# Optimization experiments

Hardware: AMD Instinct MI355X
Metric: run time of the kernel (lower is better)

The kernel has to match this reference:

```python
import jax, jax.numpy as jnp
import numpy as np

BSZ, T, ENC, HID = 128, 512, 128, 128


def setup_inputs() -> dict:
    key = jax.random.key(0)
    ks = jax.random.split(key, 8)
    encoder_output = jax.random.normal(ks[0], (BSZ, T, ENC), dtype=jnp.float32)
    lengths = jax.random.randint(ks[1], (BSZ,), 4, T + 1)
    mask = (jnp.arange(T)[None, :] < lengths[:, None]).astype(jnp.int32)
    s = 1.0 / np.sqrt(HID)  # torch LSTM init range
    W_ih = jax.random.uniform(ks[2], (4 * HID, ENC), jnp.float32, -s, s)
    W_hh = jax.random.uniform(ks[3], (4 * HID, HID), jnp.float32, -s, s)
    b_ih = jax.random.uniform(ks[4], (4 * HID,), jnp.float32, -s, s)
    b_hh = jax.random.uniform(ks[5], (4 * HID,), jnp.float32, -s, s)
    s2 = 1.0 / np.sqrt(HID + ENC)  # torch Linear init range
    fc_w = jax.random.uniform(ks[6], (1, HID + ENC), jnp.float32, -s2, s2)
    fc_b = jax.random.uniform(ks[7], (1,), jnp.float32, -s2, s2)
    return {"encoder_output": encoder_output, "mask": mask, "W_ih": W_ih,
            "W_hh": W_hh, "b_ih": b_ih, "b_hh": b_hh, "fc_w": fc_w, "fc_b": fc_b}


def _lstm_last(src, W_ih, W_hh, b_ih, b_hh):
    # src: [N, 3, E] -> last hidden state [N, H]; torch gate order i,f,g,o
    N = src.shape[0]
    H = W_hh.shape[1]
    h0 = jnp.zeros((N, H), src.dtype)
    c0 = jnp.zeros((N, H), src.dtype)

    def step(carry, x):
        h, c = carry
        gates = x @ W_ih.T + h @ W_hh.T + b_ih + b_hh
        i, f, g, o = jnp.split(gates, 4, axis=-1)
        c = jax.nn.sigmoid(f) * c + jax.nn.sigmoid(i) * jnp.tanh(g)
        h = jax.nn.sigmoid(o) * jnp.tanh(c)
        return (h, c), None

    (h, _), _ = jax.lax.scan(step, (h0, c0), jnp.swapaxes(src, 0, 1))
    return h


def reference(encoder_output, mask, W_ih, W_hh, b_ih, b_hh, fc_w, fc_b):
    B, Tn, E = encoder_output.shape
    H = W_hh.shape[1]
    lengths = jnp.sum(mask, axis=1)                       # [B]
    J = Tn - 3                                            # number of window starts
    # his_turn_states: encoder_output zeroed beyond each length
    states = encoder_output * mask[..., None].astype(encoder_output.dtype)
    # sliding windows of 3 consecutive turn states: [B, J, 3, E]
    src = jnp.stack([states[:, 0:J], states[:, 1:J + 1], states[:, 2:J + 2]], axis=2)
    h_last = _lstm_last(src.reshape(B * J, 3, E), W_ih, W_hh, b_ih, b_hh)
    h_last = h_last.reshape(B, J, H)                      # [B, J, H]
    # con_fc(concat(h, tgt)) decomposes: w_h.h + w_e.tgt + b
    w = fc_w[0]
    a = h_last @ w[:H]                                    # [B, J]
    cterm = states @ w[H:]                                # [B, T]
    logits = a[:, :, None] + cterm[:, None, :] + fc_b[0]  # [B, J, T]
    j_idx = jnp.arange(J)
    k_idx = jnp.arange(Tn)
    valid_k = (k_idx[None, None, :] >= (j_idx[None, :, None] + 3)) & \
              (k_idx[None, None, :] < lengths[:, None, None])    # candidate mask
    valid_pair = (j_idx[None, :] <= (lengths[:, None] - 4))       # [B, J]
    neg = jnp.asarray(-1e9, logits.dtype)
    lse = jax.nn.logsumexp(jnp.where(valid_k, logits, neg), axis=-1)  # [B, J]
    pos_idx = jnp.broadcast_to((j_idx + 3)[None, :, None], (B, J, 1))
    pos = jnp.take_along_axis(logits, pos_idx, axis=2)[..., 0]        # [B, J]
    loss_pair = lse - pos                                 # CE with target index 0
    vp = valid_pair.astype(logits.dtype)
    dli_loss = jnp.sum(loss_pair * vp) / jnp.sum(vp)
    return dli_loss
```

## Files before the change

### kernel.cpp

```cpp
#include <hip/hip_runtime.h>
#include <math.h>

#define BSZ 128
#define T   512
#define E   128
#define H   128


__global__ __launch_bounds__(256) void dli_dot_kernel(
    const float* __restrict__ enc,
    const int*   __restrict__ mask,
    const float* __restrict__ fc_w,
    float*       __restrict__ cterm)
{
    const int t    = threadIdx.x;
    const int wid  = t >> 6;
    const int lane = t & 63;
    const int sub  = lane >> 5;
    const int li   = lane & 31;
    const long row = (long)blockIdx.x * 8 + wid * 2 + sub;

    if (mask[row] == 0) return;

    const float4 w4 = *reinterpret_cast<const float4*>(fc_w + H + 4 * li);
    const float4 v  = *reinterpret_cast<const float4*>(enc + row * E + 4 * li);
    float p = v.x * w4.x + v.y * w4.y + v.z * w4.z + v.w * w4.w;
    #pragma unroll
    for (int off = 16; off >= 1; off >>= 1)
        p += __shfl_xor(p, off);
    if (li == 0) cterm[row] = p;
}

__global__ __launch_bounds__(T) void dli_scan_kernel(
    const float* __restrict__ cterm,
    const int*   __restrict__ mask,
    double*      __restrict__ accum,
    int*         __restrict__ scan_done,
    float*       __restrict__ out)
{
    const int b    = blockIdx.x;
    const int t    = threadIdx.x;
    const int lane = t & 63;
    const int wid  = t >> 6;

    __shared__ float s_c[T];
    __shared__ float s_a[T];
    __shared__ float s_b[T];
    __shared__ float s_red[8];
    __shared__ int   s_len;

    if (t == 0) s_len = 0;
    __syncthreads();

    const int mv = mask[b * T + t];
    unsigned long long bal = __ballot(mv != 0);
    if (lane == 0) atomicAdd(&s_len, __popcll(bal));

    s_c[t] = mv ? cterm[b * T + t] : 0.0f;
    __syncthreads();
    const int len = s_len;

    float mval = (t >= 3 && t < len) ? s_c[t] : -INFINITY;
    #pragma unroll
    for (int off = 32; off >= 1; off >>= 1)
        mval = fmaxf(mval, __shfl_xor(mval, off));
    if (lane == 0) s_red[wid] = mval;
    __syncthreads();
    if (t == 0) {
        float m = s_red[0];
        #pragma unroll
        for (int i = 1; i < 8; i++) m = fmaxf(m, s_red[i]);
        s_red[0] = m;
    }
    __syncthreads();
    const float Mrow = s_red[0];

    s_a[t] = (t >= 3 && t < len) ? expf(s_c[t] - Mrow) : 0.0f;
    __syncthreads();
    float* cur = s_a;
    float* nxt = s_b;
    #pragma unroll
    for (int d = 1; d < T; d <<= 1) {
        nxt[t] = cur[t] + ((t + d < T) ? cur[t + d] : 0.0f);
        float* tmp = cur; cur = nxt; nxt = tmp;
        __syncthreads();
    }

    float term = 0.0f;
    if (t >= 3 && t < len)
        term = Mrow + logf(cur[t]) - s_c[t];
    #pragma unroll
    for (int off = 32; off >= 1; off >>= 1)
        term += __shfl_xor(term, off);
    if (lane == 0) s_red[wid] = term;
    __syncthreads();

    if (t == 0) {
        float rs = 0.0f;
        #pragma unroll
        for (int i = 0; i < 8; i++) rs += s_red[i];
        int cnt = len - 3; if (cnt < 0) cnt = 0;
        atomicAdd(&accum[0], (double)rs);
        atomicAdd(&accum[1], (double)cnt);
        __threadfence();
        int old = atomicAdd(scan_done, 1);
        if (old == BSZ - 1) {
            __threadfence();
            double a0 = atomicAdd(&accum[0], 0.0);
            double a1 = atomicAdd(&accum[1], 0.0);
            out[0] = (float)(a0 / a1);
        }
    }
}

extern "C" void kernel_launch(void* const* d_in, const int* in_sizes, int n_in,
                              void* d_out, int out_size, void* d_ws, size_t ws_size,
                              hipStream_t stream) {
    const float* enc  = (const float*)d_in[0];
    const int*   mask = (const int*)d_in[1];
    const float* fc_w = (const float*)d_in[6];

    double* accum     = (double*)d_ws;
    int*    scan_done = (int*)((char*)d_ws + 16);
    float*  cterm     = (float*)((char*)d_ws + 1024);

    hipMemsetAsync(d_ws, 0, 32, stream);

    dli_dot_kernel<<<(BSZ * T) / 8, 256, 0, stream>>>(enc, mask, fc_w, cterm);
    dli_scan_kernel<<<BSZ, T, 0, stream>>>(cterm, mask, accum, scan_done,
                                           (float*)d_out);
}
```

Baseline: 95.76 us.

## Fuse dot-product and scan kernels into a single per-batch kernel

```diff
diff --git a/kernel.cpp b/kernel.cpp
--- a/kernel.cpp
+++ b/kernel.cpp
@@ -7,58 +7,68 @@
 #define H   128
 
 
-__global__ __launch_bounds__(256) void dli_dot_kernel(
+__global__ __launch_bounds__(512) void dli_fused_kernel(
     const float* __restrict__ enc,
     const int*   __restrict__ mask,
     const float* __restrict__ fc_w,
-    float*       __restrict__ cterm)
-{
-    const int t    = threadIdx.x;
-    const int wid  = t >> 6;
-    const int lane = t & 63;
-    const int sub  = lane >> 5;
-    const int li   = lane & 31;
-    const long row = (long)blockIdx.x * 8 + wid * 2 + sub;
-
-    if (mask[row] == 0) return;
-
-    const float4 w4 = *reinterpret_cast<const float4*>(fc_w + H + 4 * li);
-    const float4 v  = *reinterpret_cast<const float4*>(enc + row * E + 4 * li);
-    float p = v.x * w4.x + v.y * w4.y + v.z * w4.z + v.w * w4.w;
-    #pragma unroll
-    for (int off = 16; off >= 1; off >>= 1)
-        p += __shfl_xor(p, off);
-    if (li == 0) cterm[row] = p;
-}
-
-__global__ __launch_bounds__(T) void dli_scan_kernel(
-    const float* __restrict__ cterm,
-    const int*   __restrict__ mask,
-    double*      __restrict__ accum,
-    int*         __restrict__ scan_done,
     float*       __restrict__ out)
 {
     const int b    = blockIdx.x;
     const int t    = threadIdx.x;
     const int lane = t & 63;
     const int wid  = t >> 6;
+    const int hw   = t >> 5;
+    const int li   = t & 31;
 
     __shared__ float s_c[T];
     __shared__ float s_a[T];
     __shared__ float s_b[T];
+    __shared__ int   s_len[BSZ];
     __shared__ float s_red[8];
-    __shared__ int   s_len;
+    __shared__ float s_scalar[2];
 
-    if (t == 0) s_len = 0;
+    for (int j = 0; j < 16; ++j) {
+        const int r = wid * 16 + j;
+        const int* mrow = mask + r * T;
+        int s = 0;
+        #pragma unroll
+        for (int k = 0; k < 8; ++k) s += mrow[lane + k * 64];
+        #pragma unroll
+        for (int off = 32; off >= 1; off >>= 1) s += __shfl_xor(s, off);
+        if (lane == 0) s_len[r] = s;
+    }
     __syncthreads();
 
-    const int mv = mask[b * T + t];
-    unsigned long long bal = __ballot(mv != 0);
-    if (lane == 0) atomicAdd(&s_len, __popcll(bal));
+    {
+        int v = (t < BSZ) ? (s_len[t] - 3) : 0;
+        if (v < 0) v = 0;
+        #pragma unroll
+        for (int off = 32; off >= 1; off >>= 1) v += __shfl_xor(v, off);
+        if (lane == 0) s_red[wid] = (float)v;
+    }
+    __syncthreads();
+    if (t == 0) {
+        float d = 0.0f;
+        #pragma unroll
+        for (int i = 0; i < 8; ++i) d += s_red[i];
+        s_scalar[0] = d;
+    }
+    __syncthreads();
+    const int   len   = s_len[b];
+    const float denom = s_scalar[0];
 
-    s_c[t] = mv ? cterm[b * T + t] : 0.0f;
+    const float4 w4 = *reinterpret_cast<const float4*>(fc_w + H + 4 * li);
+    const float* erow = enc + (long)b * T * E;
+    #pragma unroll 4
+    for (int it = 0; it < 32; ++it) {
+        const int r = it * 16 + hw;
+        const float4 v = *reinterpret_cast<const float4*>(erow + (long)r * E + 4 * li);
+        float p = v.x * w4.x + v.y * w4.y + v.z * w4.z + v.w * w4.w;
+        #pragma unroll
+        for (int off = 16; off >= 1; off >>= 1) p += __shfl_xor(p, off);
+        if (li == 0) s_c[r] = p;
+    }
     __syncthreads();
-    const int len = s_len;
 
     float mval = (t >= 3 && t < len) ? s_c[t] : -INFINITY;
     #pragma unroll
@@ -69,11 +79,11 @@
     if (t == 0) {
         float m = s_red[0];
         #pragma unroll
-        for (int i = 1; i < 8; i++) m = fmaxf(m, s_red[i]);
-        s_red[0] = m;
+        for (int i = 1; i < 8; ++i) m = fmaxf(m, s_red[i]);
+        s_scalar[1] = m;
     }
     __syncthreads();
-    const float Mrow = s_red[0];
+    const float Mrow = s_scalar[1];
 
     s_a[t] = (t >= 3 && t < len) ? expf(s_c[t] - Mrow) : 0.0f;
     __syncthreads();
@@ -98,18 +108,8 @@
     if (t == 0) {
         float rs = 0.0f;
         #pragma unroll
-        for (int i = 0; i < 8; i++) rs += s_red[i];
-        int cnt = len - 3; if (cnt < 0) cnt = 0;
-        atomicAdd(&accum[0], (double)rs);
-        atomicAdd(&accum[1], (double)cnt);
-        __threadfence();
-        int old = atomicAdd(scan_done, 1);
-        if (old == BSZ - 1) {
-            __threadfence();
-            double a0 = atomicAdd(&accum[0], 0.0);
-            double a1 = atomicAdd(&accum[1], 0.0);
-            out[0] = (float)(a0 / a1);
-        }
+        for (int i = 0; i < 8; ++i) rs += s_red[i];
+        atomicAdd(out, rs / denom);
     }
 }
 
@@ -120,13 +120,7 @@
     const int*   mask = (const int*)d_in[1];
     const float* fc_w = (const float*)d_in[6];
 
-    double* accum     = (double*)d_ws;
-    int*    scan_done = (int*)((char*)d_ws + 16);
-    float*  cterm     = (float*)((char*)d_ws + 1024);
+    hipMemsetAsync(d_out, 0, 4, stream);
 
-    hipMemsetAsync(d_ws, 0, 32, stream);
-
-    dli_dot_kernel<<<(BSZ * T) / 8, 256, 0, stream>>>(enc, mask, fc_w, cterm);
-    dli_scan_kernel<<<BSZ, T, 0, stream>>>(cterm, mask, accum, scan_done,
-                                           (float*)d_out);
+    dli_fused_kernel<<<BSZ, T, 0, stream>>>(enc, mask, fc_w, (float*)d_out);
 }
```

New measurement: 105.3 us. 10.0% more time.

## Replace shared-memory suffix scan with wave shuffle scan and drop memset launch

Applied to the files above, without the earlier changes.

```diff
diff --git a/kernel.cpp b/kernel.cpp
--- a/kernel.cpp
+++ b/kernel.cpp
@@ -11,15 +11,23 @@
     const float* __restrict__ enc,
     const int*   __restrict__ mask,
     const float* __restrict__ fc_w,
-    float*       __restrict__ cterm)
+    float*       __restrict__ cterm,
+    double*      __restrict__ accum,
+    int*         __restrict__ scan_done)
 {
-    const int t    = threadIdx.x;
+    const int t = threadIdx.x;
+    if (blockIdx.x == 0 && t == 0) {
+        accum[0] = 0.0;
+        accum[1] = 0.0;
+        *scan_done = 0;
+    }
     const int wid  = t >> 6;
     const int lane = t & 63;
     const int sub  = lane >> 5;
     const int li   = lane & 31;
     const long row = (long)blockIdx.x * 8 + wid * 2 + sub;
 
+    if ((row & (T - 1)) < 3) return;
     if (mask[row] == 0) return;
 
     const float4 w4 = *reinterpret_cast<const float4*>(fc_w + H + 4 * li);
@@ -44,23 +52,23 @@
     const int wid  = t >> 6;
 
     __shared__ float s_c[T];
-    __shared__ float s_a[T];
-    __shared__ float s_b[T];
     __shared__ float s_red[8];
-    __shared__ int   s_len;
-
-    if (t == 0) s_len = 0;
-    __syncthreads();
+    __shared__ int   s_lw[8];
+    __shared__ float s_M;
 
     const int mv = mask[b * T + t];
     unsigned long long bal = __ballot(mv != 0);
-    if (lane == 0) atomicAdd(&s_len, __popcll(bal));
-
+    if (lane == 0) s_lw[wid] = __popcll(bal);
     s_c[t] = mv ? cterm[b * T + t] : 0.0f;
     __syncthreads();
-    const int len = s_len;
 
-    float mval = (t >= 3 && t < len) ? s_c[t] : -INFINITY;
+    int len = 0;
+    #pragma unroll
+    for (int i = 0; i < 8; ++i) len += s_lw[i];
+
+    const bool act = (t >= 3 && t < len);
+
+    float mval = act ? s_c[t] : -INFINITY;
     #pragma unroll
     for (int off = 32; off >= 1; off >>= 1)
         mval = fmaxf(mval, __shfl_xor(mval, off));
@@ -69,26 +77,25 @@
     if (t == 0) {
         float m = s_red[0];
         #pragma unroll
-        for (int i = 1; i < 8; i++) m = fmaxf(m, s_red[i]);
-        s_red[0] = m;
+        for (int i = 1; i < 8; ++i) m = fmaxf(m, s_red[i]);
+        s_M = m;
     }
     __syncthreads();
-    const float Mrow = s_red[0];
+    const float Mrow = s_M;
 
-    s_a[t] = (t >= 3 && t < len) ? expf(s_c[t] - Mrow) : 0.0f;
+    float x = act ? expf(s_c[t] - Mrow) : 0.0f;
+    #pragma unroll
+    for (int off = 1; off < 64; off <<= 1) {
+        float y = __shfl_down(x, off);
+        if (lane + off < 64) x += y;
+    }
+    if (lane == 0) s_red[wid] = x;
     __syncthreads();
-    float* cur = s_a;
-    float* nxt = s_b;
-    #pragma unroll
-    for (int d = 1; d < T; d <<= 1) {
-        nxt[t] = cur[t] + ((t + d < T) ? cur[t + d] : 0.0f);
-        float* tmp = cur; cur = nxt; nxt = tmp;
-        __syncthreads();
-    }
+    float tail = 0.0f;
+    for (int w = wid + 1; w < 8; ++w) tail += s_red[w];
+    float term = act ? (Mrow + logf(x + tail) - s_c[t]) : 0.0f;
+    __syncthreads();
 
-    float term = 0.0f;
-    if (t >= 3 && t < len)
-        term = Mrow + logf(cur[t]) - s_c[t];
     #pragma unroll
     for (int off = 32; off >= 1; off >>= 1)
         term += __shfl_xor(term, off);
@@ -98,7 +105,7 @@
     if (t == 0) {
         float rs = 0.0f;
         #pragma unroll
-        for (int i = 0; i < 8; i++) rs += s_red[i];
+        for (int i = 0; i < 8; ++i) rs += s_red[i];
         int cnt = len - 3; if (cnt < 0) cnt = 0;
         atomicAdd(&accum[0], (double)rs);
         atomicAdd(&accum[1], (double)cnt);
@@ -124,9 +131,8 @@
     int*    scan_done = (int*)((char*)d_ws + 16);
     float*  cterm     = (float*)((char*)d_ws + 1024);
 
-    hipMemsetAsync(d_ws, 0, 32, stream);
-
-    dli_dot_kernel<<<(BSZ * T) / 8, 256, 0, stream>>>(enc, mask, fc_w, cterm);
+    dli_dot_kernel<<<(BSZ * T) / 8, 256, 0, stream>>>(enc, mask, fc_w, cterm,
+                                                      accum, scan_done);
     dli_scan_kernel<<<BSZ, T, 0, stream>>>(cterm, mask, accum, scan_done,
                                            (float*)d_out);
 }
```

Result: no change. 96.00 us (+0.2%).
